# Optimization experiments

Measured on AMD Instinct MI355X. Metric: run time of the kernel, lower is better.

## Reference

```python
import jax, jax.numpy as jnp
import numpy as np

EMB = 1024
HEADS = 16
HEAD_DIM = EMB // HEADS
B, S = 4, 2048


def setup_inputs() -> dict:
    key = jax.random.key(0)
    ks = jax.random.split(key, 7)
    sc = 1.0 / np.sqrt(EMB)
    return {
        "query": jax.random.normal(ks[0], (B, S, EMB), jnp.float32),
        "key": jax.random.normal(ks[1], (B, S, EMB), jnp.float32),
        "value": jax.random.normal(ks[2], (B, S, EMB), jnp.float32),
        "Wq": jax.random.normal(ks[3], (EMB, EMB), jnp.float32) * sc,
        "Wk": jax.random.normal(ks[4], (EMB, EMB), jnp.float32) * sc,
        "Wv": jax.random.normal(ks[5], (EMB, EMB), jnp.float32) * sc,
        "Wo": jax.random.normal(ks[6], (EMB, EMB), jnp.float32) * sc,
    }


def reference(query, key, value, Wq, Wk, Wv, Wo):
    # nn.Linear applies x @ W^T; W stored as [out, in]
    def split_heads(x):  # [B,S,E] -> [B,H,S,D]
        return x.reshape(B, -1, HEADS, HEAD_DIM).transpose(0, 2, 1, 3)

    q = split_heads(query @ Wq.T)
    k = split_heads(key @ Wk.T)
    v = split_heads(value @ Wv.T)
    scores = jnp.einsum('bhse,bhte->bhst', q, k) / np.sqrt(HEAD_DIM).astype(np.float32)
    attn = jax.nn.softmax(scores, axis=-1)
    ctx = jnp.einsum('bhst,bhtd->bshd', attn, v)  # [B,S,H,D]
    out = ctx.reshape(B, -1, EMB) @ Wo.T
    return out
```

## Files before the change

kernel.cpp:

```cpp
#include <hip/hip_runtime.h>
#include <hip/hip_bf16.h>

#define EMB   1024
#define HEADS 16
#define HDIM  64
#define BB    4
#define SS    2048
#define MROWS (BB*SS)

typedef __bf16 bf16_t;
typedef __bf16 bf16x4_t __attribute__((ext_vector_type(4)));
typedef __bf16 bf16x8   __attribute__((ext_vector_type(8)));
typedef float  f32x4    __attribute__((ext_vector_type(4)));

__device__ __forceinline__ void glds16(const void* g, void* l) {
  __builtin_amdgcn_global_load_lds(
      (const __attribute__((address_space(1))) void*)g,
      (__attribute__((address_space(3))) void*)l, 16, 0, 0);
}

__launch_bounds__(256)
__global__ void cast_f32_bf16(const float* __restrict__ src, bf16_t* __restrict__ dst) {
  const int i = (blockIdx.x*256 + threadIdx.x) * 8;
  const f32x4 a = *(const f32x4*)&src[i];
  const f32x4 b = *(const f32x4*)&src[i+4];
  bf16x8 r;
  r[0]=(bf16_t)a[0]; r[1]=(bf16_t)a[1]; r[2]=(bf16_t)a[2]; r[3]=(bf16_t)a[3];
  r[4]=(bf16_t)b[0]; r[5]=(bf16_t)b[1]; r[6]=(bf16_t)b[2]; r[7]=(bf16_t)b[3];
  *(bf16x8*)&dst[i] = r;
}

template <int VEPI, typename TC>
__launch_bounds__(256)
__global__ void gemm_bt(const bf16_t* __restrict__ A, const bf16_t* __restrict__ W,
                        TC* __restrict__ C, float oscale) {
  __shared__ __align__(16) bf16_t As[128*32];
  __shared__ __align__(16) bf16_t Bs[128*32];
  const int tid  = threadIdx.x;
  const int wave = tid >> 6, lane = tid & 63;
  const int quad = lane >> 4, l16 = lane & 15;
  const int wm = wave >> 1, wn = wave & 1;
  const int bm0 = blockIdx.y * 128, bn0 = blockIdx.x * 128;

  f32x4 acc[4][4] = {};

  for (int k0 = 0; k0 < EMB; k0 += 32) {
#pragma unroll
    for (int j = 0; j < 2; ++j) {
      const int i   = wave*2 + j;
      const int row = i*16 + (lane >> 2);
      const int col = (lane & 3) * 8;
      glds16(A + (size_t)(bm0 + row)*EMB + k0 + col, &As[i*512]);
      glds16(W + (size_t)(bn0 + row)*EMB + k0 + col, &Bs[i*512]);
    }
    __syncthreads();

    bf16x8 a[4], b[4];
#pragma unroll
    for (int t = 0; t < 4; ++t) {
      a[t] = *(const bf16x8*)&As[(wm*64 + t*16 + l16)*32 + quad*8];
      b[t] = *(const bf16x8*)&Bs[(wn*64 + t*16 + l16)*32 + quad*8];
    }
#pragma unroll
    for (int mt = 0; mt < 4; ++mt)
#pragma unroll
      for (int nt = 0; nt < 4; ++nt)
        acc[mt][nt] = __builtin_amdgcn_mfma_f32_16x16x32_bf16(a[mt], b[nt], acc[mt][nt], 0, 0, 0);
    __syncthreads();
  }

  if (VEPI) {
    const int bb = bm0 >> 11;
    const int T  = ((bm0 & 2047) >> 6) + wm;
    const int h  = (bn0 >> 6) + wn;
    bf16_t* base = (bf16_t*)C + ((size_t)(bb*HEADS + h)*32 + T)*4096;
#pragma unroll
    for (int ks = 0; ks < 2; ++ks)
#pragma unroll
      for (int nt = 0; nt < 4; ++nt) {
        bf16x8 v;
#pragma unroll
        for (int r = 0; r < 4; ++r) {
          v[r]     = (bf16_t)acc[2*ks][nt][r];
          v[4 + r] = (bf16_t)acc[2*ks + 1][nt][r];
        }
        *(bf16x8*)&base[((nt*2 + ks)*64 + quad*16 + l16)*8] = v;
      }
  } else {
#pragma unroll
    for (int mt = 0; mt < 4; ++mt) {
      const int row = bm0 + wm*64 + mt*16 + quad*4;
#pragma unroll
      for (int nt = 0; nt < 4; ++nt) {
        const int col = bn0 + wn*64 + nt*16 + l16;
#pragma unroll
        for (int r = 0; r < 4; ++r)
          C[(size_t)(row + r)*EMB + col] = (TC)(acc[mt][nt][r] * oscale);
      }
    }
  }
}

__launch_bounds__(256)
__global__ void attn(const bf16_t* Qp, const bf16_t* __restrict__ Kp,
                     const bf16_t* __restrict__ Vt, bf16_t* Cx) {
  __shared__ __align__(16) bf16_t Ks[2*64*32];
  __shared__ __align__(16) bf16_t Vs[4096];

  const int tid  = threadIdx.x;
  const int wave = tid >> 6, lane = tid & 63;
  const int quad = lane >> 4, l16 = lane & 15;
  const int b = blockIdx.z, h = blockIdx.y;
  const int q0 = blockIdx.x * 128;

  bf16x8 qf[2][2];
#pragma unroll
  for (int mb = 0; mb < 2; ++mb) {
    const size_t qr = (size_t)(b*SS + q0 + wave*32 + mb*16 + l16)*EMB + h*HDIM;
#pragma unroll
    for (int ks = 0; ks < 2; ++ks)
      qf[mb][ks] = *(const bf16x8*)&Qp[qr + ks*32 + quad*8];
  }

  const bf16_t* Kb = Kp + (size_t)b*SS*EMB + h*HDIM;
  const bf16_t* Vb = Vt + ((size_t)(b*HEADS + h)*32)*4096;

  f32x4 o[2][4] = {};
  float lsum[2] = {0.f, 0.f};

  for (int t0 = 0; t0 < SS; t0 += 64) {
#pragma unroll
    for (int c = 0; c < 2; ++c) {
      const int i   = wave + c*4;
      const int r   = (i & 3)*16 + (lane >> 2);
      const int col = (lane & 3)*8;
      glds16(Kb + (size_t)(t0 + r)*EMB + c*32 + col, &Ks[i*512]);
      glds16(Vb + (size_t)(t0 >> 6)*4096 + i*512 + lane*8, &Vs[i*512]);
    }
    __syncthreads();

    f32x4 st[2][4] = {};
#pragma unroll
    for (int cb = 0; cb < 4; ++cb) {
      const bf16x8 kf0 = *(const bf16x8*)&Ks[(cb*16 + l16)*32 + quad*8];
      const bf16x8 kf1 = *(const bf16x8*)&Ks[2048 + (cb*16 + l16)*32 + quad*8];
#pragma unroll
      for (int mb = 0; mb < 2; ++mb) {
        st[mb][cb] = __builtin_amdgcn_mfma_f32_16x16x32_bf16(kf0, qf[mb][0], st[mb][cb], 0, 0, 0);
        st[mb][cb] = __builtin_amdgcn_mfma_f32_16x16x32_bf16(kf1, qf[mb][1], st[mb][cb], 0, 0, 0);
      }
    }

    bf16x8 pb[2][2];
#pragma unroll
    for (int mb = 0; mb < 2; ++mb) {
      float ls = 0.f;
#pragma unroll
      for (int kb = 0; kb < 4; ++kb)
#pragma unroll
        for (int r = 0; r < 4; ++r) {
          const float p = __builtin_amdgcn_exp2f(st[mb][kb][r]);
          st[mb][kb][r] = p;
          ls += p;
        }
      lsum[mb] += ls;
#pragma unroll
      for (int ks = 0; ks < 2; ++ks)
#pragma unroll
        for (int r = 0; r < 4; ++r) {
          pb[mb][ks][r]     = (bf16_t)st[mb][2*ks][r];
          pb[mb][ks][4 + r] = (bf16_t)st[mb][2*ks + 1][r];
        }
    }

#pragma unroll
    for (int ks = 0; ks < 2; ++ks)
#pragma unroll
      for (int dt = 0; dt < 4; ++dt) {
        const bf16x8 vf = *(const bf16x8*)&Vs[((dt*2 + ks)*64 + quad*16 + l16)*8];
#pragma unroll
        for (int mb = 0; mb < 2; ++mb)
          o[mb][dt] = __builtin_amdgcn_mfma_f32_16x16x32_bf16(vf, pb[mb][ks], o[mb][dt], 0, 0, 0);
      }
    __syncthreads();
  }

#pragma unroll
  for (int mb = 0; mb < 2; ++mb) {
    float l = lsum[mb];
    l += __shfl_xor(l, 16, 64);
    l += __shfl_xor(l, 32, 64);
    const float inv = 1.0f / l;
    const size_t row = (size_t)(b*SS + q0 + wave*32 + mb*16 + l16)*EMB + h*HDIM;
#pragma unroll
    for (int dt = 0; dt < 4; ++dt) {
      bf16x4_t v;
#pragma unroll
      for (int r = 0; r < 4; ++r) v[r] = (bf16_t)(o[mb][dt][r] * inv);
      *(bf16x4_t*)&Cx[row + dt*16 + quad*4] = v;
    }
  }
}

extern "C" void kernel_launch(void* const* d_in, const int* in_sizes, int n_in,
                              void* d_out, int out_size, void* d_ws, size_t ws_size,
                              hipStream_t stream) {
  (void)in_sizes; (void)n_in; (void)out_size; (void)ws_size;
  const float* query = (const float*)d_in[0];
  const float* key   = (const float*)d_in[1];
  const float* value = (const float*)d_in[2];
  const float* WqF   = (const float*)d_in[3];
  const float* WkF   = (const float*)d_in[4];
  const float* WvF   = (const float*)d_in[5];
  const float* WoF   = (const float*)d_in[6];

  bf16_t* S1  = (bf16_t*)d_ws;
  bf16_t* S2  = S1 + (size_t)MROWS*EMB;
  bf16_t* Wqb = S2 + (size_t)MROWS*EMB;
  bf16_t* Wkb = Wqb + (size_t)EMB*EMB;
  bf16_t* Wvb = Wkb + (size_t)EMB*EMB;
  bf16_t* Wob = Wvb + (size_t)EMB*EMB;
  bf16_t* S5  = (bf16_t*)d_out;
  bf16_t* S6  = S5 + (size_t)MROWS*EMB;
  float*  out = (float*)d_out;

  const float sscale = 0.125f * 1.44269504f;

  const dim3 cw(EMB*EMB/(256*8));
  const dim3 ca((size_t)MROWS*EMB/(256*8));
  const dim3 gg(EMB/128, MROWS/128);

  cast_f32_bf16<<<cw, 256, 0, stream>>>(WqF, Wqb);
  cast_f32_bf16<<<cw, 256, 0, stream>>>(WkF, Wkb);
  cast_f32_bf16<<<cw, 256, 0, stream>>>(WvF, Wvb);
  cast_f32_bf16<<<cw, 256, 0, stream>>>(WoF, Wob);

  cast_f32_bf16<<<ca, 256, 0, stream>>>(query, S1);
  gemm_bt<0, bf16_t><<<gg, 256, 0, stream>>>(S1, Wqb, S2, sscale);

  cast_f32_bf16<<<ca, 256, 0, stream>>>(key, S1);
  gemm_bt<0, bf16_t><<<gg, 256, 0, stream>>>(S1, Wkb, S6, 1.0f);

  cast_f32_bf16<<<ca, 256, 0, stream>>>(value, S5);
  gemm_bt<1, bf16_t><<<gg, 256, 0, stream>>>(S5, Wvb, S1, 1.0f);

  attn<<<dim3(SS/128, HEADS, BB), 256, 0, stream>>>(S2, S6, S1, S2);

  gemm_bt<0, float><<<gg, 256, 0, stream>>>(S2, Wob, out, 1.0f);
}
```

Measured before the change: 372.7 us.

## Batch casts and QKV GEMMs into single launches, double attention key tile

All seven fp32→bf16 casts now run in one multi-tensor kernel, and the Q/K/V projections run as one GEMM launch that picks its operands from blockIdx.z. This cuts the number of kernel launches and lets the three projections run concurrently on the GPU instead of one after another. The attention loop now stages 128 keys per iteration, which halves the number of barriers but doubles its LDS use. If the workspace is too small, a fallback path keeps the value cast and value projection as separate launches.

```diff
diff --git a/kernel.cpp b/kernel.cpp
--- a/kernel.cpp
+++ b/kernel.cpp
@@ -17,6 +17,27 @@
   __builtin_amdgcn_global_load_lds(
       (const __attribute__((address_space(1))) void*)g,
       (__attribute__((address_space(3))) void*)l, 16, 0, 0);
+}
+
+__launch_bounds__(256)
+__global__ void cast_multi(const float* s0, const float* s1, const float* s2,
+                           const float* s3, const float* s4, const float* s5,
+                           const float* s6,
+                           bf16_t* d0, bf16_t* d1, bf16_t* d2, bf16_t* d3,
+                           bf16_t* d4, bf16_t* d5, bf16_t* d6, int nact) {
+  const int z = blockIdx.z;
+  if (z >= nact && blockIdx.x >= 512) return;
+  const float* ss[7] = {s0, s1, s2, s3, s4, s5, s6};
+  bf16_t*      dd[7] = {d0, d1, d2, d3, d4, d5, d6};
+  const float* s = ss[z];
+  bf16_t*      d = dd[z];
+  const int i = (blockIdx.x*256 + threadIdx.x) * 8;
+  const f32x4 a = *(const f32x4*)&s[i];
+  const f32x4 b = *(const f32x4*)&s[i+4];
+  bf16x8 r;
+  r[0]=(bf16_t)a[0]; r[1]=(bf16_t)a[1]; r[2]=(bf16_t)a[2]; r[3]=(bf16_t)a[3];
+  r[4]=(bf16_t)b[0]; r[5]=(bf16_t)b[1]; r[6]=(bf16_t)b[2]; r[7]=(bf16_t)b[3];
+  *(bf16x8*)&d[i] = r;
 }
 
 __launch_bounds__(256)
@@ -30,10 +51,45 @@
   *(bf16x8*)&dst[i] = r;
 }
 
-template <int VEPI, typename TC>
-__launch_bounds__(256)
-__global__ void gemm_bt(const bf16_t* __restrict__ A, const bf16_t* __restrict__ W,
-                        TC* __restrict__ C, float oscale) {
+__device__ __forceinline__ void gemm_core(const bf16_t* __restrict__ A,
+                                          const bf16_t* __restrict__ W,
+                                          bf16_t* As, bf16_t* Bs,
+                                          f32x4 acc[4][4],
+                                          int bm0, int bn0,
+                                          int wave, int lane) {
+  const int quad = lane >> 4, l16 = lane & 15;
+  const int wm = wave >> 1, wn = wave & 1;
+  for (int k0 = 0; k0 < EMB; k0 += 32) {
+#pragma unroll
+    for (int j = 0; j < 2; ++j) {
+      const int i   = wave*2 + j;
+      const int row = i*16 + (lane >> 2);
+      const int col = (lane & 3) * 8;
+      glds16(A + (size_t)(bm0 + row)*EMB + k0 + col, &As[i*512]);
+      glds16(W + (size_t)(bn0 + row)*EMB + k0 + col, &Bs[i*512]);
+    }
+    __syncthreads();
+
+    bf16x8 a[4], b[4];
+#pragma unroll
+    for (int t = 0; t < 4; ++t) {
+      a[t] = *(const bf16x8*)&As[(wm*64 + t*16 + l16)*32 + quad*8];
+      b[t] = *(const bf16x8*)&Bs[(wn*64 + t*16 + l16)*32 + quad*8];
+    }
+#pragma unroll
+    for (int mt = 0; mt < 4; ++mt)
+#pragma unroll
+      for (int nt = 0; nt < 4; ++nt)
+        acc[mt][nt] = __builtin_amdgcn_mfma_f32_16x16x32_bf16(a[mt], b[nt], acc[mt][nt], 0, 0, 0);
+    __syncthreads();
+  }
+}
+
+__launch_bounds__(256)
+__global__ void gemm_qkv(const bf16_t* A0, const bf16_t* A1, const bf16_t* A2,
+                         const bf16_t* W0, const bf16_t* W1, const bf16_t* W2,
+                         bf16_t* C0, bf16_t* C1, bf16_t* C2,
+                         float sscale, int zbase) {
   __shared__ __align__(16) bf16_t As[128*32];
   __shared__ __align__(16) bf16_t Bs[128*32];
   const int tid  = threadIdx.x;
@@ -41,39 +97,21 @@
   const int quad = lane >> 4, l16 = lane & 15;
   const int wm = wave >> 1, wn = wave & 1;
   const int bm0 = blockIdx.y * 128, bn0 = blockIdx.x * 128;
+  const int z = blockIdx.z + zbase;
+
+  const bf16_t* A = (z == 0) ? A0 : (z == 1) ? A1 : A2;
+  const bf16_t* W = (z == 0) ? W0 : (z == 1) ? W1 : W2;
+  bf16_t*       C = (z == 0) ? C0 : (z == 1) ? C1 : C2;
+  const float oscale = (z == 0) ? sscale : 1.0f;
 
   f32x4 acc[4][4] = {};
-
-  for (int k0 = 0; k0 < EMB; k0 += 32) {
-#pragma unroll
-    for (int j = 0; j < 2; ++j) {
-      const int i   = wave*2 + j;
-      const int row = i*16 + (lane >> 2);
-      const int col = (lane & 3) * 8;
-      glds16(A + (size_t)(bm0 + row)*EMB + k0 + col, &As[i*512]);
-      glds16(W + (size_t)(bn0 + row)*EMB + k0 + col, &Bs[i*512]);
-    }
-    __syncthreads();
-
-    bf16x8 a[4], b[4];
-#pragma unroll
-    for (int t = 0; t < 4; ++t) {
-      a[t] = *(const bf16x8*)&As[(wm*64 + t*16 + l16)*32 + quad*8];
-      b[t] = *(const bf16x8*)&Bs[(wn*64 + t*16 + l16)*32 + quad*8];
-    }
-#pragma unroll
-    for (int mt = 0; mt < 4; ++mt)
-#pragma unroll
-      for (int nt = 0; nt < 4; ++nt)
-        acc[mt][nt] = __builtin_amdgcn_mfma_f32_16x16x32_bf16(a[mt], b[nt], acc[mt][nt], 0, 0, 0);
-    __syncthreads();
-  }
-
-  if (VEPI) {
+  gemm_core(A, W, As, Bs, acc, bm0, bn0, wave, lane);
+
+  if (z == 2) {
     const int bb = bm0 >> 11;
     const int T  = ((bm0 & 2047) >> 6) + wm;
     const int h  = (bn0 >> 6) + wn;
-    bf16_t* base = (bf16_t*)C + ((size_t)(bb*HEADS + h)*32 + T)*4096;
+    bf16_t* base = C + ((size_t)(bb*HEADS + h)*32 + T)*4096;
 #pragma unroll
     for (int ks = 0; ks < 2; ++ks)
 #pragma unroll
@@ -95,8 +133,35 @@
         const int col = bn0 + wn*64 + nt*16 + l16;
 #pragma unroll
         for (int r = 0; r < 4; ++r)
-          C[(size_t)(row + r)*EMB + col] = (TC)(acc[mt][nt][r] * oscale);
-      }
+          C[(size_t)(row + r)*EMB + col] = (bf16_t)(acc[mt][nt][r] * oscale);
+      }
+    }
+  }
+}
+
+__launch_bounds__(256)
+__global__ void gemm_out(const bf16_t* __restrict__ A, const bf16_t* __restrict__ W,
+                         float* __restrict__ C) {
+  __shared__ __align__(16) bf16_t As[128*32];
+  __shared__ __align__(16) bf16_t Bs[128*32];
+  const int tid  = threadIdx.x;
+  const int wave = tid >> 6, lane = tid & 63;
+  const int quad = lane >> 4, l16 = lane & 15;
+  const int wm = wave >> 1, wn = wave & 1;
+  const int bm0 = blockIdx.y * 128, bn0 = blockIdx.x * 128;
+
+  f32x4 acc[4][4] = {};
+  gemm_core(A, W, As, Bs, acc, bm0, bn0, wave, lane);
+
+#pragma unroll
+  for (int mt = 0; mt < 4; ++mt) {
+    const int row = bm0 + wm*64 + mt*16 + quad*4;
+#pragma unroll
+    for (int nt = 0; nt < 4; ++nt) {
+      const int col = bn0 + wn*64 + nt*16 + l16;
+#pragma unroll
+      for (int r = 0; r < 4; ++r)
+        C[(size_t)(row + r)*EMB + col] = acc[mt][nt][r];
     }
   }
 }
@@ -104,8 +169,8 @@
 __launch_bounds__(256)
 __global__ void attn(const bf16_t* Qp, const bf16_t* __restrict__ Kp,
                      const bf16_t* __restrict__ Vt, bf16_t* Cx) {
-  __shared__ __align__(16) bf16_t Ks[2*64*32];
-  __shared__ __align__(16) bf16_t Vs[4096];
+  __shared__ __align__(16) bf16_t Ks[2*4096];
+  __shared__ __align__(16) bf16_t Vs[2*4096];
 
   const int tid  = threadIdx.x;
   const int wave = tid >> 6, lane = tid & 63;
@@ -128,60 +193,68 @@
   f32x4 o[2][4] = {};
   float lsum[2] = {0.f, 0.f};
 
-  for (int t0 = 0; t0 < SS; t0 += 64) {
-#pragma unroll
-    for (int c = 0; c < 2; ++c) {
-      const int i   = wave + c*4;
-      const int r   = (i & 3)*16 + (lane >> 2);
-      const int col = (lane & 3)*8;
-      glds16(Kb + (size_t)(t0 + r)*EMB + c*32 + col, &Ks[i*512]);
-      glds16(Vb + (size_t)(t0 >> 6)*4096 + i*512 + lane*8, &Vs[i*512]);
-    }
+  for (int t0 = 0; t0 < SS; t0 += 128) {
+#pragma unroll
+    for (int sub = 0; sub < 2; ++sub)
+#pragma unroll
+      for (int c = 0; c < 2; ++c) {
+        const int i   = wave + c*4;
+        const int r   = (i & 3)*16 + (lane >> 2);
+        const int col = (lane & 3)*8;
+        glds16(Kb + (size_t)(t0 + sub*64 + r)*EMB + c*32 + col, &Ks[sub*4096 + i*512]);
+        glds16(Vb + (size_t)((t0 >> 6) + sub)*4096 + i*512 + lane*8, &Vs[sub*4096 + i*512]);
+      }
     __syncthreads();
 
-    f32x4 st[2][4] = {};
-#pragma unroll
-    for (int cb = 0; cb < 4; ++cb) {
-      const bf16x8 kf0 = *(const bf16x8*)&Ks[(cb*16 + l16)*32 + quad*8];
-      const bf16x8 kf1 = *(const bf16x8*)&Ks[2048 + (cb*16 + l16)*32 + quad*8];
+#pragma unroll
+    for (int sub = 0; sub < 2; ++sub) {
+      const bf16_t* Kss = &Ks[sub*4096];
+      const bf16_t* Vss = &Vs[sub*4096];
+
+      f32x4 st[2][4] = {};
+#pragma unroll
+      for (int cb = 0; cb < 4; ++cb) {
+        const bf16x8 kf0 = *(const bf16x8*)&Kss[(cb*16 + l16)*32 + quad*8];
+        const bf16x8 kf1 = *(const bf16x8*)&Kss[2048 + (cb*16 + l16)*32 + quad*8];
+#pragma unroll
+        for (int mb = 0; mb < 2; ++mb) {
+          st[mb][cb] = __builtin_amdgcn_mfma_f32_16x16x32_bf16(kf0, qf[mb][0], st[mb][cb], 0, 0, 0);
+          st[mb][cb] = __builtin_amdgcn_mfma_f32_16x16x32_bf16(kf1, qf[mb][1], st[mb][cb], 0, 0, 0);
+        }
+      }
+
+      bf16x8 pb[2][2];
 #pragma unroll
       for (int mb = 0; mb < 2; ++mb) {
-        st[mb][cb] = __builtin_amdgcn_mfma_f32_16x16x32_bf16(kf0, qf[mb][0], st[mb][cb], 0, 0, 0);
-        st[mb][cb] = __builtin_amdgcn_mfma_f32_16x16x32_bf16(kf1, qf[mb][1], st[mb][cb], 0, 0, 0);
-      }
-    }
-
-    bf16x8 pb[2][2];
-#pragma unroll
-    for (int mb = 0; mb < 2; ++mb) {
-      float ls = 0.f;
-#pragma unroll
-      for (int kb = 0; kb < 4; ++kb)
-#pragma unroll
-        for (int r = 0; r < 4; ++r) {
-          const float p = __builtin_amdgcn_exp2f(st[mb][kb][r]);
-          st[mb][kb][r] = p;
-          ls += p;
+        float ls = 0.f;
+#pragma unroll
+        for (int kb = 0; kb < 4; ++kb)
+#pragma unroll
+          for (int r = 0; r < 4; ++r) {
+            const float p = __builtin_amdgcn_exp2f(st[mb][kb][r]);
+            st[mb][kb][r] = p;
+            ls += p;
+          }
+        lsum[mb] += ls;
+#pragma unroll
+        for (int ks = 0; ks < 2; ++ks)
+#pragma unroll
+          for (int r = 0; r < 4; ++r) {
+            pb[mb][ks][r]     = (bf16_t)st[mb][2*ks][r];
+            pb[mb][ks][4 + r] = (bf16_t)st[mb][2*ks + 1][r];
+          }
+      }
+
+#pragma unroll
+      for (int ks = 0; ks < 2; ++ks)
+#pragma unroll
+        for (int dt = 0; dt < 4; ++dt) {
+          const bf16x8 vf = *(const bf16x8*)&Vss[((dt*2 + ks)*64 + quad*16 + l16)*8];
+#pragma unroll
+          for (int mb = 0; mb < 2; ++mb)
+            o[mb][dt] = __builtin_amdgcn_mfma_f32_16x16x32_bf16(vf, pb[mb][ks], o[mb][dt], 0, 0, 0);
         }
-      lsum[mb] += ls;
-#pragma unroll
-      for (int ks = 0; ks < 2; ++ks)
-#pragma unroll
-        for (int r = 0; r < 4; ++r) {
-          pb[mb][ks][r]     = (bf16_t)st[mb][2*ks][r];
-          pb[mb][ks][4 + r] = (bf16_t)st[mb][2*ks + 1][r];
-        }
-    }
-
-#pragma unroll
-    for (int ks = 0; ks < 2; ++ks)
-#pragma unroll
-      for (int dt = 0; dt < 4; ++dt) {
-        const bf16x8 vf = *(const bf16x8*)&Vs[((dt*2 + ks)*64 + quad*16 + l16)*8];
-#pragma unroll
-        for (int mb = 0; mb < 2; ++mb)
-          o[mb][dt] = __builtin_amdgcn_mfma_f32_16x16x32_bf16(vf, pb[mb][ks], o[mb][dt], 0, 0, 0);
-      }
+    }
     __syncthreads();
   }
 
@@ -205,7 +278,7 @@
 extern "C" void kernel_launch(void* const* d_in, const int* in_sizes, int n_in,
                               void* d_out, int out_size, void* d_ws, size_t ws_size,
                               hipStream_t stream) {
-  (void)in_sizes; (void)n_in; (void)out_size; (void)ws_size;
+  (void)in_sizes; (void)n_in; (void)out_size;
   const float* query = (const float*)d_in[0];
   const float* key   = (const float*)d_in[1];
   const float* value = (const float*)d_in[2];
@@ -214,37 +287,54 @@
   const float* WvF   = (const float*)d_in[5];
   const float* WoF   = (const float*)d_in[6];
 
-  bf16_t* S1  = (bf16_t*)d_ws;
-  bf16_t* S2  = S1 + (size_t)MROWS*EMB;
-  bf16_t* Wqb = S2 + (size_t)MROWS*EMB;
-  bf16_t* Wkb = Wqb + (size_t)EMB*EMB;
-  bf16_t* Wvb = Wkb + (size_t)EMB*EMB;
-  bf16_t* Wob = Wvb + (size_t)EMB*EMB;
-  bf16_t* S5  = (bf16_t*)d_out;
-  bf16_t* S6  = S5 + (size_t)MROWS*EMB;
-  float*  out = (float*)d_out;
+  const size_t AN = (size_t)MROWS*EMB;
+  const size_t WN = (size_t)EMB*EMB;
+  float* out = (float*)d_out;
+  bf16_t* S5 = (bf16_t*)d_out;
+  bf16_t* S6 = S5 + AN;
 
   const float sscale = 0.125f * 1.44269504f;
 
-  const dim3 cw(EMB*EMB/(256*8));
-  const dim3 ca((size_t)MROWS*EMB/(256*8));
-  const dim3 gg(EMB/128, MROWS/128);
-
-  cast_f32_bf16<<<cw, 256, 0, stream>>>(WqF, Wqb);
-  cast_f32_bf16<<<cw, 256, 0, stream>>>(WkF, Wkb);
-  cast_f32_bf16<<<cw, 256, 0, stream>>>(WvF, Wvb);
-  cast_f32_bf16<<<cw, 256, 0, stream>>>(WoF, Wob);
-
-  cast_f32_bf16<<<ca, 256, 0, stream>>>(query, S1);
-  gemm_bt<0, bf16_t><<<gg, 256, 0, stream>>>(S1, Wqb, S2, sscale);
-
-  cast_f32_bf16<<<ca, 256, 0, stream>>>(key, S1);
-  gemm_bt<0, bf16_t><<<gg, 256, 0, stream>>>(S1, Wkb, S6, 1.0f);
-
-  cast_f32_bf16<<<ca, 256, 0, stream>>>(value, S5);
-  gemm_bt<1, bf16_t><<<gg, 256, 0, stream>>>(S5, Wvb, S1, 1.0f);
-
-  attn<<<dim3(SS/128, HEADS, BB), 256, 0, stream>>>(S2, S6, S1, S2);
-
-  gemm_bt<0, float><<<gg, 256, 0, stream>>>(S2, Wob, out, 1.0f);
-}
+  const dim3 gqkv(EMB/128, MROWS/128, 3);
+  const dim3 gqk (EMB/128, MROWS/128, 2);
+  const dim3 gv  (EMB/128, MROWS/128, 1);
+  const dim3 gg  (EMB/128, MROWS/128);
+  const dim3 gattn(SS/128, HEADS, BB);
+
+  if (ws_size >= (size_t)(4*AN + 4*WN) * sizeof(bf16_t)) {
+    bf16_t* qb  = (bf16_t*)d_ws;
+    bf16_t* kb  = qb + AN;
+    bf16_t* vb  = kb + AN;
+    bf16_t* S2  = vb + AN;
+    bf16_t* Wqb = S2 + AN;
+    bf16_t* Wkb = Wqb + WN;
+    bf16_t* Wvb = Wkb + WN;
+    bf16_t* Wob = Wvb + WN;
+
+    cast_multi<<<dim3(AN/2048, 1, 7), 256, 0, stream>>>(
+        query, key, value, WqF, WkF, WvF, WoF,
+        qb, kb, vb, Wqb, Wkb, Wvb, Wob, 3);
+    gemm_qkv<<<gqkv, 256, 0, stream>>>(qb, kb, vb, Wqb, Wkb, Wvb,
+                                       S2, S6, S5, sscale, 0);
+    attn<<<gattn, 256, 0, stream>>>(S2, S6, S5, S2);
+    gemm_out<<<gg, 256, 0, stream>>>(S2, Wob, out);
+  } else {
+    bf16_t* S1  = (bf16_t*)d_ws;
+    bf16_t* S2  = S1 + AN;
+    bf16_t* Wqb = S2 + AN;
+    bf16_t* Wkb = Wqb + WN;
+    bf16_t* Wvb = Wkb + WN;
+    bf16_t* Wob = Wvb + WN;
+
+    cast_multi<<<dim3(AN/2048, 1, 6), 256, 0, stream>>>(
+        query, key, WqF, WkF, WvF, WoF, WoF,
+        S1, S5, Wqb, Wkb, Wvb, Wob, Wob, 2);
+    gemm_qkv<<<gqk, 256, 0, stream>>>(S1, S5, S1, Wqb, Wkb, Wvb,
+                                      S2, S6, S5, sscale, 0);
+    cast_f32_bf16<<<dim3(AN/2048), 256, 0, stream>>>(value, S1);
+    gemm_qkv<<<gv, 256, 0, stream>>>(S1, S1, S1, Wvb, Wvb, Wvb,
+                                     S5, S5, S5, 1.0f, 2);
+    attn<<<gattn, 256, 0, stream>>>(S2, S6, S5, S2);
+    gemm_out<<<gg, 256, 0, stream>>>(S2, Wob, out);
+  }
+}
```

Result: faster. 365.1 us (-2.0%).
